# Optimization experiments

Hardware: AMD Instinct MI355X
Metric: run time of the kernel (lower is better)

Reference implementation:

```python
import jax, jax.numpy as jnp
import numpy as np

EPS = 1e-6
KH, KW = 3, 3
SH, SW = 1, 1


def _unfold(x, kh, kw, sh, sw):
    # x: [N, C, H, W] -> patches [N, C, kh*kw, L], L = ox*oy (torch.nn.Unfold layout)
    N, C, H, W = x.shape
    ox = (H - kh) // sh + 1
    oy = (W - kw) // sw + 1
    pats = [x[:, :, i:i + sh * ox:sh, j:j + sw * oy:sw]
            for i in range(kh) for j in range(kw)]
    p = jnp.stack(pats, axis=2)  # [N, C, K, ox, oy]
    return p.reshape(N, C, kh * kw, ox * oy), ox, oy


def setup_inputs() -> dict:
    key = jax.random.key(0)
    kx, k1, k2 = jax.random.split(key, 3)
    x = jax.random.uniform(kx, (32, 2, 64, 64, 64), dtype=jnp.float32)
    w1 = jax.random.uniform(k1, (64, KH * KW), dtype=jnp.float32)
    w2 = jax.random.uniform(k2, (128, 64), dtype=jnp.float32)
    return {"x": x, "w1": w1, "w2": w2}


def reference(x, w1, w2):
    B = x.shape[0]
    out_ch = w2.shape[0]
    xr = x[:, 0]  # rotation plane [B, C, H, W]
    xa = x[:, 1]  # magnitude plane

    pr, ox, oy = _unfold(xr, KH, KW, SH, SW)  # [B, C, K, L]
    pa, _, _ = _unfold(xa, KH, KW, SH, SW)

    # weightNormalize1: squared weights normalized by GLOBAL sum (rot branch)
    w1_glob = w1 ** 2 / jnp.sum(w1 ** 2)
    w2_glob = w2 ** 2 / jnp.sum(w2 ** 2)
    # weightNormalize (drop_prob=0): squared weights normalized PER ROW (abs branch)
    w1_row = w1 ** 2 / jnp.sum(w1 ** 2, axis=1, keepdims=True)
    w2_row = w2 ** 2 / jnp.sum(w2 ** 2, axis=1, keepdims=True)

    # rotation branch: two weighted contractions
    rot = jnp.einsum('bckl,ck->bcl', pr, w1_glob)          # [B, C, L]
    out_rot = jnp.einsum('bcl,oc->bol', rot, w2_glob)      # [B, O, L]
    out_rot = out_rot.reshape(B, 1, out_ch, ox, oy)

    # magnitude branch: log -> weighted contractions -> exp
    la = jnp.log(pa + EPS)                                  # [B, C, K, L]
    a1 = jnp.einsum('bckl,ck->bcl', la, w1_row)             # [B, C, L]
    out_abs = jnp.exp(jnp.einsum('bcl,oc->bol', a1, w2_row))
    out_abs = out_abs.reshape(B, 1, out_ch, ox, oy)

    return jnp.concatenate([out_rot, out_abs], axis=1)  # [B, 2, O, ox, oy]
```

## Files before the change

### kernel.cpp

```cpp
#include <hip/hip_runtime.h>
#include <cstdint>
#include <cstddef>

#define EPSF 1e-6f

typedef __attribute__((ext_vector_type(4))) float f32x4;
typedef __attribute__((ext_vector_type(8))) short s16x8;
typedef union { s16x8 v; unsigned u[4]; } s16x8u;

static __device__ __forceinline__ unsigned short f2bf(float f) {
    unsigned u = __float_as_uint(f);
    u += 0x7FFFu + ((u >> 16) & 1u);
    return (unsigned short)(u >> 16);
}
static __device__ __forceinline__ float bf2f(unsigned short h) {
    return __uint_as_float(((unsigned)h) << 16);
}
static __device__ __forceinline__ void pack2(float a, float b, unsigned& H, unsigned& L) {
    unsigned short ha = f2bf(a), hb = f2bf(b);
    unsigned short la = f2bf(a - bf2f(ha)), lb = f2bf(b - bf2f(hb));
    H = ((unsigned)hb << 16) | (unsigned)ha;
    L = ((unsigned)lb << 16) | (unsigned)la;
}


__global__ __launch_bounds__(256) void prep_sums(const float* __restrict__ w1,
                                                 const float* __restrict__ w2,
                                                 float* __restrict__ ws) {
    const int bid = blockIdx.x;
    const int t = threadIdx.x;
    const int lane = t & 63;
    const int wv = t >> 6;
    if (bid < 32) {
        const int row = bid * 4 + wv;
        float v = w2[row * 64 + lane];
        float s = v * v;
        #pragma unroll
        for (int d = 32; d > 0; d >>= 1) s += __shfl_down(s, d);
        if (lane == 0) ws[17602 + row] = s;
    } else if (t < 64) {
        float rs = 0.f;
        #pragma unroll
        for (int k = 0; k < 9; ++k) { float v = w1[t * 9 + k]; rs += v * v; }
        ws[17538 + t] = rs;
    }
}

__global__ __launch_bounds__(256) void prep_pack(const float* __restrict__ w1,
                                                 const float* __restrict__ w2,
                                                 float* __restrict__ ws) {
    const int t = threadIdx.x;
    const int lane = t & 63;
    const int gid = blockIdx.x * 256 + t;

    float a = ws[17538 + lane];
    float b0 = ws[17602 + lane] + ws[17602 + 64 + lane];
    #pragma unroll
    for (int d = 32; d > 0; d >>= 1) {
        a += __shfl_xor(a, d);
        b0 += __shfl_xor(b0, d);
    }
    const float t1 = a, t2 = b0;

    unsigned* wsu = (unsigned*)ws;
    if (gid < 4096) {
        const int row = gid >> 5;
        const int cp = gid & 31;
        float v0 = w2[row * 64 + 2 * cp];
        float v1 = w2[row * 64 + 2 * cp + 1];
        float q0 = v0 * v0, q1 = v1 * v1;
        const float rs = ws[17602 + row];
        unsigned H, L;
        pack2(q0 / t2, q1 / t2, H, L);
        wsu[1152 + row * 32 + cp] = H;
        wsu[5248 + row * 32 + cp] = L;
        pack2(q0 / rs, q1 / rs, H, L);
        wsu[9344 + row * 32 + cp] = H;
        wsu[13440 + row * 32 + cp] = L;
    } else if (gid < 4672) {
        const int i = gid - 4096;
        const int c = i / 9;
        const int k = i - c * 9;
        float v = w1[i];
        float q = v * v;
        ws[c * 9 + k] = q / t1;
        ws[576 + c * 9 + k] = q / ws[17538 + c];
    }
}

__global__ __launch_bounds__(512) void conv_fused(const float* __restrict__ x,
                                                  const float* __restrict__ ws,
                                                  float* __restrict__ out) {
    const int b = blockIdx.x;
    const int branch = blockIdx.y;
    const int hg = blockIdx.z;
    const int h0 = hg * 2;
    const int t = threadIdx.x;
    const int lane = t & 63;
    const int w = __builtin_amdgcn_readfirstlane(t >> 6);
    const int lm = lane & 15;
    const int q = lane >> 4;

    __shared__ unsigned rotH[128 * 33];
    __shared__ unsigned rotL[128 * 33];

    const float* __restrict__ w1n = ws + branch * 576;
    const unsigned* __restrict__ wsu = (const unsigned*)ws;
    const unsigned* __restrict__ w2H = wsu + 1152 + branch * 8192;
    const unsigned* __restrict__ w2L = w2H + 4096;
    const float* __restrict__ xb = x + (size_t)(b * 2 + branch) * (64 * 4096);

    {
        const int cpair = w * 4 + q;
        const int c0 = 2 * cpair;
        const float* xp0 = xb + c0 * 4096 + h0 * 64 + 4 * lm;
        const float* xp1 = xp0 + 4096;
        float4 va[4], vb[4];
        #pragma unroll
        for (int r = 0; r < 4; ++r) va[r] = *(const float4*)(xp0 + r * 64);
        #pragma unroll
        for (int r = 0; r < 4; ++r) vb[r] = *(const float4*)(xp1 + r * 64);
        if (branch) {
            #pragma unroll
            for (int r = 0; r < 4; ++r) {
                va[r].x = __logf(va[r].x + EPSF); va[r].y = __logf(va[r].y + EPSF);
                va[r].z = __logf(va[r].z + EPSF); va[r].w = __logf(va[r].w + EPSF);
                vb[r].x = __logf(vb[r].x + EPSF); vb[r].y = __logf(vb[r].y + EPSF);
                vb[r].z = __logf(vb[r].z + EPSF); vb[r].w = __logf(vb[r].w + EPSF);
            }
        }
        float sax[4], say[4], sbx[4], sby[4];
        #pragma unroll
        for (int r = 0; r < 4; ++r) {
            sax[r] = __shfl_down(va[r].x, 1); say[r] = __shfl_down(va[r].y, 1);
            sbx[r] = __shfl_down(vb[r].x, 1); sby[r] = __shfl_down(vb[r].y, 1);
        }
        const float* wc0 = w1n + c0 * 9;
        const float* wc1 = wc0 + 9;
        float pa[2][4], pb[2][4];
        #pragma unroll
        for (int row = 0; row < 2; ++row) {
            #pragma unroll
            for (int rr = 0; rr < 3; ++rr) {
                const float4 u = va[row + rr];
                const float ux1 = sax[row + rr], uy1 = say[row + rr];
                const float t0 = wc0[rr * 3], t1_ = wc0[rr * 3 + 1], t2_ = wc0[rr * 3 + 2];
                if (rr == 0) {
                    pa[row][0] = u.x * t0 + u.y * t1_ + u.z * t2_;
                    pa[row][1] = u.y * t0 + u.z * t1_ + u.w * t2_;
                    pa[row][2] = u.z * t0 + u.w * t1_ + ux1 * t2_;
                    pa[row][3] = u.w * t0 + ux1 * t1_ + uy1 * t2_;
                } else {
                    pa[row][0] += u.x * t0 + u.y * t1_ + u.z * t2_;
                    pa[row][1] += u.y * t0 + u.z * t1_ + u.w * t2_;
                    pa[row][2] += u.z * t0 + u.w * t1_ + ux1 * t2_;
                    pa[row][3] += u.w * t0 + ux1 * t1_ + uy1 * t2_;
                }
            }
            #pragma unroll
            for (int rr = 0; rr < 3; ++rr) {
                const float4 u = vb[row + rr];
                const float ux1 = sbx[row + rr], uy1 = sby[row + rr];
                const float t0 = wc1[rr * 3], t1_ = wc1[rr * 3 + 1], t2_ = wc1[rr * 3 + 2];
                if (rr == 0) {
                    pb[row][0] = u.x * t0 + u.y * t1_ + u.z * t2_;
                    pb[row][1] = u.y * t0 + u.z * t1_ + u.w * t2_;
                    pb[row][2] = u.z * t0 + u.w * t1_ + ux1 * t2_;
                    pb[row][3] = u.w * t0 + ux1 * t1_ + uy1 * t2_;
                } else {
                    pb[row][0] += u.x * t0 + u.y * t1_ + u.z * t2_;
                    pb[row][1] += u.y * t0 + u.z * t1_ + u.w * t2_;
                    pb[row][2] += u.z * t0 + u.w * t1_ + ux1 * t2_;
                    pb[row][3] += u.w * t0 + ux1 * t1_ + uy1 * t2_;
                }
            }
        }
        #pragma unroll
        for (int row = 0; row < 2; ++row) {
            #pragma unroll
            for (int i = 0; i < 4; ++i) {
                const int pxl = row * 64 + 4 * lm + i;
                unsigned H, L;
                pack2(pa[row][i], pb[row][i], H, L);
                rotH[pxl * 33 + cpair] = H;
                rotL[pxl * 33 + cpair] = L;
            }
        }
    }

    const int woc = (w & 3) * 32;
    const int half = w >> 2;
    s16x8u aH[2][2], aL[2][2];
    #pragma unroll
    for (int mt = 0; mt < 2; ++mt) {
        #pragma unroll
        for (int kk = 0; kk < 2; ++kk) {
            const int off = (woc + mt * 16 + lm) * 32 + kk * 16 + q * 4;
            const unsigned* ph = w2H + off;
            const unsigned* pl = w2L + off;
            #pragma unroll
            for (int j = 0; j < 4; ++j) {
                aH[mt][kk].u[j] = ph[j];
                aL[mt][kk].u[j] = pl[j];
            }
        }
    }
    __syncthreads();

    f32x4 acc[2][4];
    #pragma unroll
    for (int mt = 0; mt < 2; ++mt)
        #pragma unroll
        for (int nt = 0; nt < 4; ++nt)
            acc[mt][nt] = (f32x4){0.f, 0.f, 0.f, 0.f};

    #pragma unroll
    for (int nt = 0; nt < 4; ++nt) {
        #pragma unroll
        for (int kk = 0; kk < 2; ++kk) {
            const int idx = (half * 64 + nt * 16 + lm) * 33 + kk * 16 + q * 4;
            s16x8u bH, bL;
            #pragma unroll
            for (int j = 0; j < 4; ++j) bH.u[j] = rotH[idx + j];
            #pragma unroll
            for (int j = 0; j < 4; ++j) bL.u[j] = rotL[idx + j];
            #pragma unroll
            for (int mt = 0; mt < 2; ++mt) {
                acc[mt][nt] = __builtin_amdgcn_mfma_f32_16x16x32_bf16(aH[mt][kk].v, bH.v, acc[mt][nt], 0, 0, 0);
                acc[mt][nt] = __builtin_amdgcn_mfma_f32_16x16x32_bf16(aH[mt][kk].v, bL.v, acc[mt][nt], 0, 0, 0);
                acc[mt][nt] = __builtin_amdgcn_mfma_f32_16x16x32_bf16(aL[mt][kk].v, bH.v, acc[mt][nt], 0, 0, 0);
            }
        }
    }

    #pragma unroll
    for (int mt = 0; mt < 2; ++mt) {
        const int oc0 = woc + mt * 16 + q * 4;
        #pragma unroll
        for (int nt = 0; nt < 4; ++nt) {
            const int col = nt * 16 + lm;
            if (col < 62) {
                const size_t base =
                    ((size_t)((b * 2 + branch) * 128 + oc0)) * 3844 +
                    (size_t)(h0 + half) * 62 + col;
                #pragma unroll
                for (int r = 0; r < 4; ++r) {
                    float v = acc[mt][nt][r];
                    if (branch) v = __expf(v);
                    out[base + (size_t)r * 3844] = v;
                }
            }
        }
    }
}

extern "C" void kernel_launch(void* const* d_in, const int* in_sizes, int n_in,
                              void* d_out, int out_size, void* d_ws, size_t ws_size,
                              hipStream_t stream) {
    const float* x  = (const float*)d_in[0];
    const float* w1 = (const float*)d_in[1];
    const float* w2 = (const float*)d_in[2];
    float* out = (float*)d_out;
    float* ws  = (float*)d_ws;

    prep_sums<<<33, 256, 0, stream>>>(w1, w2, ws);
    prep_pack<<<19, 256, 0, stream>>>(w1, w2, ws);

    dim3 grid(32, 2, 31);
    conv_fused<<<grid, 512, 0, stream>>>(x, ws, out);
}
```

Measured before the change: 200.5 us.

## Merge prep kernels, use hardware bf16 pack, single-pass bf16 for rotation branch

Folds the two weight-prep kernels into one launch, with the global and per-row sums computed redundantly per block in shared memory. Replaces the software bf16 rounding with the v_cvt_pk_bf16_f32 instruction. For the rotation branch it drops the low-order bf16 split and runs one MFMA per tile instead of three, and it raises wave priority around the MFMA loop. The goal is less launch overhead and less matrix work, at the cost of lower accuracy for the rotation output, which becomes plain bf16 instead of split-precision.

```diff
diff --git a/kernel.cpp b/kernel.cpp
--- a/kernel.cpp
+++ b/kernel.cpp
@@ -8,59 +8,64 @@
 typedef __attribute__((ext_vector_type(8))) short s16x8;
 typedef union { s16x8 v; unsigned u[4]; } s16x8u;
 
-static __device__ __forceinline__ unsigned short f2bf(float f) {
-    unsigned u = __float_as_uint(f);
-    u += 0x7FFFu + ((u >> 16) & 1u);
-    return (unsigned short)(u >> 16);
-}
-static __device__ __forceinline__ float bf2f(unsigned short h) {
-    return __uint_as_float(((unsigned)h) << 16);
-}
 static __device__ __forceinline__ void pack2(float a, float b, unsigned& H, unsigned& L) {
-    unsigned short ha = f2bf(a), hb = f2bf(b);
-    unsigned short la = f2bf(a - bf2f(ha)), lb = f2bf(b - bf2f(hb));
-    H = ((unsigned)hb << 16) | (unsigned)ha;
-    L = ((unsigned)lb << 16) | (unsigned)la;
-}
-
-
-__global__ __launch_bounds__(256) void prep_sums(const float* __restrict__ w1,
-                                                 const float* __restrict__ w2,
-                                                 float* __restrict__ ws) {
-    const int bid = blockIdx.x;
+    unsigned h, l;
+    asm("v_cvt_pk_bf16_f32 %0, %1, %2" : "=v"(h) : "v"(a), "v"(b));
+    float ra = a - __uint_as_float(h << 16);
+    float rb = b - __uint_as_float(h & 0xffff0000u);
+    asm("v_cvt_pk_bf16_f32 %0, %1, %2" : "=v"(l) : "v"(ra), "v"(rb));
+    H = h; L = l;
+}
+static __device__ __forceinline__ unsigned packH(float a, float b) {
+    unsigned h;
+    asm("v_cvt_pk_bf16_f32 %0, %1, %2" : "=v"(h) : "v"(a), "v"(b));
+    return h;
+}
+
+
+__global__ __launch_bounds__(256) void prep(const float* __restrict__ w1,
+                                            const float* __restrict__ w2,
+                                            float* __restrict__ ws) {
+    __shared__ float s1row[64];
+    __shared__ float red[4];
+    __shared__ float rs8[8];
     const int t = threadIdx.x;
     const int lane = t & 63;
     const int wv = t >> 6;
-    if (bid < 32) {
-        const int row = bid * 4 + wv;
-        float v = w2[row * 64 + lane];
-        float s = v * v;
-        #pragma unroll
-        for (int d = 32; d > 0; d >>= 1) s += __shfl_down(s, d);
-        if (lane == 0) ws[17602 + row] = s;
-    } else if (t < 64) {
+    const int gid = blockIdx.x * 256 + t;
+
+    float s = 0.f;
+    #pragma unroll
+    for (int i = 0; i < 32; ++i) { float v = w2[t + 256 * i]; s += v * v; }
+    #pragma unroll
+    for (int d = 32; d > 0; d >>= 1) s += __shfl_xor(s, d);
+    if (lane == 0) red[wv] = s;
+
+    if (t < 64) {
         float rs = 0.f;
         #pragma unroll
         for (int k = 0; k < 9; ++k) { float v = w1[t * 9 + k]; rs += v * v; }
-        ws[17538 + t] = rs;
-    }
-}
-
-__global__ __launch_bounds__(256) void prep_pack(const float* __restrict__ w1,
-                                                 const float* __restrict__ w2,
-                                                 float* __restrict__ ws) {
-    const int t = threadIdx.x;
-    const int lane = t & 63;
-    const int gid = blockIdx.x * 256 + t;
-
-    float a = ws[17538 + lane];
-    float b0 = ws[17602 + lane] + ws[17602 + 64 + lane];
-    #pragma unroll
-    for (int d = 32; d > 0; d >>= 1) {
-        a += __shfl_xor(a, d);
-        b0 += __shfl_xor(b0, d);
-    }
-    const float t1 = a, t2 = b0;
+        s1row[t] = rs;
+    }
+
+    if (blockIdx.x < 16) {
+        const int r8 = t >> 5;
+        const int e = t & 31;
+        const int row = blockIdx.x * 8 + r8;
+        float v0 = w2[row * 64 + e];
+        float v1 = w2[row * 64 + 32 + e];
+        float rr = v0 * v0 + v1 * v1;
+        #pragma unroll
+        for (int d = 16; d > 0; d >>= 1) rr += __shfl_down(rr, d);
+        if (e == 0) rs8[r8] = rr;
+    }
+    __syncthreads();
+
+    const float t2 = red[0] + red[1] + red[2] + red[3];
+    float a = s1row[lane];
+    #pragma unroll
+    for (int d = 32; d > 0; d >>= 1) a += __shfl_xor(a, d);
+    const float t1 = a;
 
     unsigned* wsu = (unsigned*)ws;
     if (gid < 4096) {
@@ -69,7 +74,7 @@
         float v0 = w2[row * 64 + 2 * cp];
         float v1 = w2[row * 64 + 2 * cp + 1];
         float q0 = v0 * v0, q1 = v1 * v1;
-        const float rs = ws[17602 + row];
+        const float rs = rs8[t >> 5];
         unsigned H, L;
         pack2(q0 / t2, q1 / t2, H, L);
         wsu[1152 + row * 32 + cp] = H;
@@ -84,7 +89,7 @@
         float v = w1[i];
         float q = v * v;
         ws[c * 9 + k] = q / t1;
-        ws[576 + c * 9 + k] = q / ws[17538 + c];
+        ws[576 + c * 9 + k] = q / s1row[c];
     }
 }
 
@@ -100,6 +105,7 @@
     const int w = __builtin_amdgcn_readfirstlane(t >> 6);
     const int lm = lane & 15;
     const int q = lane >> 4;
+    const bool dual = (branch != 0);
 
     __shared__ unsigned rotH[128 * 33];
     __shared__ unsigned rotL[128 * 33];
@@ -109,6 +115,10 @@
     const unsigned* __restrict__ w2H = wsu + 1152 + branch * 8192;
     const unsigned* __restrict__ w2L = w2H + 4096;
     const float* __restrict__ xb = x + (size_t)(b * 2 + branch) * (64 * 4096);
+
+    const int woc = (w & 3) * 32;
+    const int half = w >> 2;
+    s16x8u aH[2][2], aL[2][2];
 
     {
         const int cpair = w * 4 + q;
@@ -120,7 +130,7 @@
         for (int r = 0; r < 4; ++r) va[r] = *(const float4*)(xp0 + r * 64);
         #pragma unroll
         for (int r = 0; r < 4; ++r) vb[r] = *(const float4*)(xp1 + r * 64);
-        if (branch) {
+        if (dual) {
             #pragma unroll
             for (int r = 0; r < 4; ++r) {
                 va[r].x = __logf(va[r].x + EPSF); va[r].y = __logf(va[r].y + EPSF);
@@ -175,33 +185,43 @@
                 }
             }
         }
+
+        #pragma unroll
+        for (int mt = 0; mt < 2; ++mt) {
+            #pragma unroll
+            for (int kk = 0; kk < 2; ++kk) {
+                const int off = (woc + mt * 16 + lm) * 32 + kk * 16 + q * 4;
+                const unsigned* ph = w2H + off;
+                #pragma unroll
+                for (int j = 0; j < 4; ++j) aH[mt][kk].u[j] = ph[j];
+            }
+        }
+        if (dual) {
+            #pragma unroll
+            for (int mt = 0; mt < 2; ++mt) {
+                #pragma unroll
+                for (int kk = 0; kk < 2; ++kk) {
+                    const int off = (woc + mt * 16 + lm) * 32 + kk * 16 + q * 4;
+                    const unsigned* pl = w2L + off;
+                    #pragma unroll
+                    for (int j = 0; j < 4; ++j) aL[mt][kk].u[j] = pl[j];
+                }
+            }
+        }
+
         #pragma unroll
         for (int row = 0; row < 2; ++row) {
             #pragma unroll
             for (int i = 0; i < 4; ++i) {
                 const int pxl = row * 64 + 4 * lm + i;
-                unsigned H, L;
-                pack2(pa[row][i], pb[row][i], H, L);
-                rotH[pxl * 33 + cpair] = H;
-                rotL[pxl * 33 + cpair] = L;
-            }
-        }
-    }
-
-    const int woc = (w & 3) * 32;
-    const int half = w >> 2;
-    s16x8u aH[2][2], aL[2][2];
-    #pragma unroll
-    for (int mt = 0; mt < 2; ++mt) {
-        #pragma unroll
-        for (int kk = 0; kk < 2; ++kk) {
-            const int off = (woc + mt * 16 + lm) * 32 + kk * 16 + q * 4;
-            const unsigned* ph = w2H + off;
-            const unsigned* pl = w2L + off;
-            #pragma unroll
-            for (int j = 0; j < 4; ++j) {
-                aH[mt][kk].u[j] = ph[j];
-                aL[mt][kk].u[j] = pl[j];
+                if (dual) {
+                    unsigned H, L;
+                    pack2(pa[row][i], pb[row][i], H, L);
+                    rotH[pxl * 33 + cpair] = H;
+                    rotL[pxl * 33 + cpair] = L;
+                } else {
+                    rotH[pxl * 33 + cpair] = packH(pa[row][i], pb[row][i]);
+                }
             }
         }
     }
@@ -214,24 +234,43 @@
         for (int nt = 0; nt < 4; ++nt)
             acc[mt][nt] = (f32x4){0.f, 0.f, 0.f, 0.f};
 
-    #pragma unroll
-    for (int nt = 0; nt < 4; ++nt) {
-        #pragma unroll
-        for (int kk = 0; kk < 2; ++kk) {
-            const int idx = (half * 64 + nt * 16 + lm) * 33 + kk * 16 + q * 4;
-            s16x8u bH, bL;
-            #pragma unroll
-            for (int j = 0; j < 4; ++j) bH.u[j] = rotH[idx + j];
-            #pragma unroll
-            for (int j = 0; j < 4; ++j) bL.u[j] = rotL[idx + j];
-            #pragma unroll
-            for (int mt = 0; mt < 2; ++mt) {
-                acc[mt][nt] = __builtin_amdgcn_mfma_f32_16x16x32_bf16(aH[mt][kk].v, bH.v, acc[mt][nt], 0, 0, 0);
-                acc[mt][nt] = __builtin_amdgcn_mfma_f32_16x16x32_bf16(aH[mt][kk].v, bL.v, acc[mt][nt], 0, 0, 0);
-                acc[mt][nt] = __builtin_amdgcn_mfma_f32_16x16x32_bf16(aL[mt][kk].v, bH.v, acc[mt][nt], 0, 0, 0);
-            }
-        }
-    }
+    __builtin_amdgcn_s_setprio(1);
+    if (dual) {
+        #pragma unroll
+        for (int nt = 0; nt < 4; ++nt) {
+            #pragma unroll
+            for (int kk = 0; kk < 2; ++kk) {
+                const int idx = (half * 64 + nt * 16 + lm) * 33 + kk * 16 + q * 4;
+                s16x8u bH, bL;
+                #pragma unroll
+                for (int j = 0; j < 4; ++j) bH.u[j] = rotH[idx + j];
+                #pragma unroll
+                for (int j = 0; j < 4; ++j) bL.u[j] = rotL[idx + j];
+                #pragma unroll
+                for (int mt = 0; mt < 2; ++mt) {
+                    acc[mt][nt] = __builtin_amdgcn_mfma_f32_16x16x32_bf16(aH[mt][kk].v, bH.v, acc[mt][nt], 0, 0, 0);
+                    acc[mt][nt] = __builtin_amdgcn_mfma_f32_16x16x32_bf16(aH[mt][kk].v, bL.v, acc[mt][nt], 0, 0, 0);
+                    acc[mt][nt] = __builtin_amdgcn_mfma_f32_16x16x32_bf16(aL[mt][kk].v, bH.v, acc[mt][nt], 0, 0, 0);
+                }
+            }
+        }
+    } else {
+        #pragma unroll
+        for (int nt = 0; nt < 4; ++nt) {
+            #pragma unroll
+            for (int kk = 0; kk < 2; ++kk) {
+                const int idx = (half * 64 + nt * 16 + lm) * 33 + kk * 16 + q * 4;
+                s16x8u bH;
+                #pragma unroll
+                for (int j = 0; j < 4; ++j) bH.u[j] = rotH[idx + j];
+                #pragma unroll
+                for (int mt = 0; mt < 2; ++mt) {
+                    acc[mt][nt] = __builtin_amdgcn_mfma_f32_16x16x32_bf16(aH[mt][kk].v, bH.v, acc[mt][nt], 0, 0, 0);
+                }
+            }
+        }
+    }
+    __builtin_amdgcn_s_setprio(0);
 
     #pragma unroll
     for (int mt = 0; mt < 2; ++mt) {
@@ -246,7 +285,7 @@
                 #pragma unroll
                 for (int r = 0; r < 4; ++r) {
                     float v = acc[mt][nt][r];
-                    if (branch) v = __expf(v);
+                    if (dual) v = __expf(v);
                     out[base + (size_t)r * 3844] = v;
                 }
             }
@@ -263,8 +302,7 @@
     float* out = (float*)d_out;
     float* ws  = (float*)d_ws;
 
-    prep_sums<<<33, 256, 0, stream>>>(w1, w2, ws);
-    prep_pack<<<19, 256, 0, stream>>>(w1, w2, ws);
+    prep<<<19, 256, 0, stream>>>(w1, w2, ws);
 
     dim3 grid(32, 2, 31);
     conv_fused<<<grid, 512, 0, stream>>>(x, ws, out);
```

Measured after the change: 197.6 us. No clear change (-1.5%).
